# Optimization experiments

Measured on AMD Instinct MI355X. Metric: run time of the kernel, lower is better.

Reference implementation:

```python
import jax, jax.numpy as jnp
import numpy as np

EARLY_ROUND = 6
LATE_ROUND = 12
NUM_CLASSES = 35


def setup_inputs() -> dict:
    key = jax.random.key(0)
    k1, k2, k3 = jax.random.split(key, 3)
    B = 1048576
    logits = jax.random.normal(k1, (B, NUM_CLASSES), dtype=jnp.float32)
    targets = jax.random.randint(k2, (B,), 0, NUM_CLASSES, dtype=jnp.int64)
    turns = jax.random.randint(k3, (B,), 0, 24, dtype=jnp.int64)
    return {"logits": logits, "targets": targets, "turns": turns}


def reference(logits, targets, turns):
    # per-sample cross entropy (reduction='none')
    logp = jax.nn.log_softmax(logits, axis=-1)  # [B, C]
    losses = -jnp.take_along_axis(logp, targets[:, None], axis=-1)[:, 0]  # [B]
    # piecewise-linear weight: 0.7 for turn<=early, 1.0 for turn>=late, lerp between
    t = turns.astype(logits.dtype)
    frac = (t - EARLY_ROUND) / (LATE_ROUND - EARLY_ROUND)
    weights = jnp.clip(0.7 + 0.3 * frac, 0.7, 1.0)
    return jnp.mean(losses * weights)
```

## Files before the change

### kernel.cpp

```cpp
#include <hip/hip_runtime.h>
#include <math.h>

#define NUM_CLASSES 35
#define ROWS_PER_BLOCK 256

__global__ __launch_bounds__(256) void fuzzy_loss_pass1(
    const float* __restrict__ logits,
    const int* __restrict__ targets,
    const int* __restrict__ turns,
    float* __restrict__ block_sums)
{
    __shared__ float lds[ROWS_PER_BLOCK * NUM_CLASSES];
    const int tid  = threadIdx.x;
    const int row0 = blockIdx.x * ROWS_PER_BLOCK;

    {
        const float4* src = (const float4*)(logits + (size_t)row0 * NUM_CLASSES);
        float4* dst = (float4*)lds;
        const int nvec = ROWS_PER_BLOCK * NUM_CLASSES / 4;
        #pragma unroll
        for (int i = 0; i < nvec / ROWS_PER_BLOCK; ++i)
            dst[tid + i * ROWS_PER_BLOCK] = src[tid + i * ROWS_PER_BLOCK];
        {
            int j = 8 * ROWS_PER_BLOCK + tid;
            if (tid < nvec - 8 * ROWS_PER_BLOCK) dst[j] = src[j];
        }
    }
    __syncthreads();

    const int row = row0 + tid;
    const float* r = lds + tid * NUM_CLASSES;

    float s = 0.0f;
    #pragma unroll
    for (int j = 0; j < NUM_CLASSES; ++j) s += __expf(r[j]);

    const int tgt = targets[row];
    const float xt = r[tgt];
    float loss = __logf(s) - xt;

    const float t = (float)turns[row];
    float w = fmaf(0.05f, t, 0.4f);
    w = fminf(fmaxf(w, 0.7f), 1.0f);
    float v = loss * w;

    #pragma unroll
    for (int off = 32; off > 0; off >>= 1)
        v += __shfl_down(v, off, 64);

    __shared__ float wsum[ROWS_PER_BLOCK / 64];
    if ((tid & 63) == 0) wsum[tid >> 6] = v;
    __syncthreads();
    if (tid == 0)
        block_sums[blockIdx.x] = wsum[0] + wsum[1] + wsum[2] + wsum[3];
}

__global__ __launch_bounds__(256) void fuzzy_loss_pass2(
    const float* __restrict__ block_sums,
    float* __restrict__ out,
    int nblocks, float inv_B)
{
    const int tid = threadIdx.x;
    float v = 0.0f;
    const float4* src = (const float4*)block_sums;
    for (int i = tid; i < nblocks / 4; i += 256) {
        float4 f = src[i];
        v += (f.x + f.y) + (f.z + f.w);
    }
    #pragma unroll
    for (int off = 32; off > 0; off >>= 1)
        v += __shfl_down(v, off, 64);

    __shared__ float wsum[4];
    if ((tid & 63) == 0) wsum[tid >> 6] = v;
    __syncthreads();
    if (tid == 0)
        out[0] = (wsum[0] + wsum[1] + wsum[2] + wsum[3]) * inv_B;
}

extern "C" void kernel_launch(void* const* d_in, const int* in_sizes, int n_in,
                              void* d_out, int out_size, void* d_ws, size_t ws_size,
                              hipStream_t stream) {
    const float* logits  = (const float*)d_in[0];
    const int*   targets = (const int*)d_in[1];
    const int*   turns   = (const int*)d_in[2];
    float*       out     = (float*)d_out;
    float*       partial = (float*)d_ws;

    const int B = in_sizes[1];
    const int blocks = B / ROWS_PER_BLOCK;

    fuzzy_loss_pass1<<<blocks, ROWS_PER_BLOCK, 0, stream>>>(logits, targets, turns, partial);
    fuzzy_loss_pass2<<<1, 256, 0, stream>>>(partial, out, blocks, 1.0f / (float)B);
}
```

Measured before the change: 213.1 us.

## Fuse final reduction into main kernel via last-block atomic counter

Merges the two-kernel reduction into one launch: each block stores its partial sum and bumps a global atomic counter, and the last block to finish sums all partials and writes the mean. It also issues the target and turn loads before the LDS staging so their latency overlaps. This removes a second kernel launch and its dependency gap, at the cost of an atomic per block and a serial tail reduction done by one block. The counter is reset by the last block so repeated calls work.

```diff
diff --git a/kernel.cpp b/kernel.cpp
--- a/kernel.cpp
+++ b/kernel.cpp
@@ -4,78 +4,87 @@
 #define NUM_CLASSES 35
 #define ROWS_PER_BLOCK 256
 
-__global__ __launch_bounds__(256) void fuzzy_loss_pass1(
+__device__ unsigned int g_counter = 0;
+
+__global__ __launch_bounds__(256) void fuzzy_loss_fused(
     const float* __restrict__ logits,
     const int* __restrict__ targets,
     const int* __restrict__ turns,
-    float* __restrict__ block_sums)
+    float* __restrict__ block_sums,
+    float* __restrict__ out,
+    int nblocks, float inv_B)
 {
     __shared__ float lds[ROWS_PER_BLOCK * NUM_CLASSES];
+    __shared__ float wsum[ROWS_PER_BLOCK / 64];
+    __shared__ int   is_last;
+
     const int tid  = threadIdx.x;
     const int row0 = blockIdx.x * ROWS_PER_BLOCK;
+    const int row  = row0 + tid;
+
+    const int tgt = targets[row];
+    const int trn = turns[row];
 
     {
         const float4* src = (const float4*)(logits + (size_t)row0 * NUM_CLASSES);
         float4* dst = (float4*)lds;
-        const int nvec = ROWS_PER_BLOCK * NUM_CLASSES / 4;
         #pragma unroll
-        for (int i = 0; i < nvec / ROWS_PER_BLOCK; ++i)
+        for (int i = 0; i < 8; ++i)
             dst[tid + i * ROWS_PER_BLOCK] = src[tid + i * ROWS_PER_BLOCK];
         {
             int j = 8 * ROWS_PER_BLOCK + tid;
-            if (tid < nvec - 8 * ROWS_PER_BLOCK) dst[j] = src[j];
+            if (tid < 192) dst[j] = src[j];
         }
     }
     __syncthreads();
 
-    const int row = row0 + tid;
     const float* r = lds + tid * NUM_CLASSES;
 
     float s = 0.0f;
     #pragma unroll
     for (int j = 0; j < NUM_CLASSES; ++j) s += __expf(r[j]);
 
-    const int tgt = targets[row];
     const float xt = r[tgt];
     float loss = __logf(s) - xt;
 
-    const float t = (float)turns[row];
-    float w = fmaf(0.05f, t, 0.4f);
+    float w = fmaf(0.05f, (float)trn, 0.4f);
     w = fminf(fmaxf(w, 0.7f), 1.0f);
     float v = loss * w;
 
     #pragma unroll
     for (int off = 32; off > 0; off >>= 1)
         v += __shfl_down(v, off, 64);
-
-    __shared__ float wsum[ROWS_PER_BLOCK / 64];
     if ((tid & 63) == 0) wsum[tid >> 6] = v;
     __syncthreads();
-    if (tid == 0)
-        block_sums[blockIdx.x] = wsum[0] + wsum[1] + wsum[2] + wsum[3];
-}
 
-__global__ __launch_bounds__(256) void fuzzy_loss_pass2(
-    const float* __restrict__ block_sums,
-    float* __restrict__ out,
-    int nblocks, float inv_B)
-{
-    const int tid = threadIdx.x;
-    float v = 0.0f;
-    const float4* src = (const float4*)block_sums;
-    for (int i = tid; i < nblocks / 4; i += 256) {
-        float4 f = src[i];
-        v += (f.x + f.y) + (f.z + f.w);
+    if (tid == 0) {
+        float p = wsum[0] + wsum[1] + wsum[2] + wsum[3];
+        __hip_atomic_store(&block_sums[blockIdx.x], p,
+                           __ATOMIC_RELAXED, __HIP_MEMORY_SCOPE_AGENT);
+        unsigned old = __hip_atomic_fetch_add(&g_counter, 1u,
+                           __ATOMIC_ACQ_REL, __HIP_MEMORY_SCOPE_AGENT);
+        is_last = (old == (unsigned)(nblocks - 1));
     }
-    #pragma unroll
-    for (int off = 32; off > 0; off >>= 1)
-        v += __shfl_down(v, off, 64);
+    __syncthreads();
 
-    __shared__ float wsum[4];
-    if ((tid & 63) == 0) wsum[tid >> 6] = v;
-    __syncthreads();
-    if (tid == 0)
-        out[0] = (wsum[0] + wsum[1] + wsum[2] + wsum[3]) * inv_B;
+    if (is_last) {
+        float acc = 0.0f;
+        const float4* src = (const float4*)block_sums;
+        for (int i = tid; i < nblocks / 4; i += ROWS_PER_BLOCK) {
+            float4 f = src[i];
+            acc += (f.x + f.y) + (f.z + f.w);
+        }
+        #pragma unroll
+        for (int off = 32; off > 0; off >>= 1)
+            acc += __shfl_down(acc, off, 64);
+        if ((tid & 63) == 0) wsum[tid >> 6] = acc;
+        __syncthreads();
+        if (tid == 0) {
+            out[0] = (wsum[0] + wsum[1] + wsum[2] + wsum[3]) * inv_B;
+            __hip_atomic_store(&g_counter, 0u,
+                               __ATOMIC_RELAXED, __HIP_MEMORY_SCOPE_AGENT);
+        }
+    }
 }
 
 extern "C" void kernel_launch(void* const* d_in, const int* in_sizes, int n_in,
@@ -90,6 +99,6 @@
     const int B = in_sizes[1];
     const int blocks = B / ROWS_PER_BLOCK;
 
-    fuzzy_loss_pass1<<<blocks, ROWS_PER_BLOCK, 0, stream>>>(logits, targets, turns, partial);
-    fuzzy_loss_pass2<<<1, 256, 0, stream>>>(partial, out, blocks, 1.0f / (float)B);
+    fuzzy_loss_fused<<<blocks, ROWS_PER_BLOCK, 0, stream>>>(
+        logits, targets, turns, partial, out, blocks, 1.0f / (float)B);
 }
```

After: 370.2 us. +73.7%, slower.
